# Kernel tuning notes

Measured on AMD Instinct MI355X. Metric: run time of the kernel, lower is better.

Reference implementation:

```python
import jax, jax.numpy as jnp
import numpy as np

B, H, W, C, UNITS = 16, 64, 64, 64, 128

def setup_inputs() -> dict:
    key = jax.random.key(0)
    k1, k2 = jax.random.split(key)
    x = jax.random.normal(k1, (B, H, W, C), dtype=jnp.float32)
    # 'random_normal' keras initializer defaults to stddev=0.05
    w = jax.random.normal(k2, (UNITS, C, W, H), dtype=jnp.float32) * 0.05
    return {"x": x, "w": w}

def reference(x, w):
    # Original: transpose NHWC->NCHW, broadcasted matmul (W,H)@(H,W),
    # reduce-sum over C, transpose back, relu.
    # Fused contraction: y[b,i,j,u] = sum_{c,h} w[u,c,i,h] * x[b,h,j,c]
    y = jnp.einsum('ucih,bhjc->biju', w, x)  # (B, W, W, units)
    return jax.nn.relu(y)
```

## Files before the change

### kernel.cpp

```cpp
#include <hip/hip_runtime.h>
#include <hip/hip_bf16.h>


typedef __attribute__((ext_vector_type(4))) float f32x4;
typedef __attribute__((ext_vector_type(8))) short bf16x8;
typedef __attribute__((ext_vector_type(4))) unsigned int u32x4;
typedef __attribute__((ext_vector_type(2))) unsigned int u32x2;
typedef unsigned short ushort_t;

static __device__ __forceinline__ unsigned int cvt_pk_bf16(float lo, float hi) {
  unsigned int r;
  asm("v_cvt_pk_bf16_f32 %0, %1, %2" : "=v"(r) : "v"(lo), "v"(hi));
  return r;
}

static __device__ __forceinline__ void async_copy16(void* lds, const void* g) {
  __builtin_amdgcn_global_load_lds(
      (const __attribute__((address_space(1))) unsigned int*)g,
      (__attribute__((address_space(3))) unsigned int*)lds, 16, 0, 0);
}

__global__ __launch_bounds__(256)
void conv_x(const float* __restrict__ X, ushort_t* __restrict__ Xb, int n4) {
  int idx = blockIdx.x * 256 + threadIdx.x;
  const int stride = gridDim.x * 256;
  for (; idx < n4; idx += stride) {
    f32x4 v = ((const f32x4*)X)[idx];
    u32x2 o;
    o.x = cvt_pk_bf16(v.x, v.y);
    o.y = cvt_pk_bf16(v.z, v.w);
    ((u32x2*)Xb)[idx] = o;
  }
}

__global__ __launch_bounds__(256)
void conv_w(const float* __restrict__ W, ushort_t* __restrict__ Wb) {
  __shared__ float T[64][65];
  const int bid = blockIdx.x;
  const int u = bid >> 6;
  const int i = bid & 63;
  const int t = threadIdx.x;

  const int hq = t & 15;
  const int c4 = t >> 4;
  const float* base = W + (((size_t)u * 64) * 64 + i) * 64;
#pragma unroll
  for (int it = 0; it < 4; ++it) {
    const int c = it * 16 + c4;
    f32x4 v = *(const f32x4*)(base + (size_t)c * 4096 + hq * 4);
    *(f32x4*)&T[c][hq * 4] = v;
  }
  __syncthreads();

  const int h = t >> 2;
  const int c0 = (t & 3) * 16;
  unsigned int pk[8];
#pragma unroll
  for (int q = 0; q < 8; ++q)
    pk[q] = cvt_pk_bf16(T[c0 + 2 * q][h], T[c0 + 2 * q + 1][h]);
  ushort_t* out = Wb + (((size_t)i * 128 + u) * 64 + h) * 64 + c0;
  ((u32x4*)out)[0] = *(u32x4*)&pk[0];
  ((u32x4*)out)[1] = *(u32x4*)&pk[4];
}

__global__ __launch_bounds__(512, 1)
void gemm256(const ushort_t* __restrict__ Xb, const ushort_t* __restrict__ Wb,
             float* __restrict__ P0, float* __restrict__ P1) {
  __shared__ ushort_t As[3][256 * 32];
  __shared__ ushort_t Bs[3][256 * 32];

  const int tid = threadIdx.x;
  const int lane = tid & 63;
  const int wid = tid >> 6;
  const int wm = wid >> 2;
  const int wn = wid & 3;

  const int bid = blockIdx.x;
  const int wg = (bid & 7) * 32 + (bid >> 3);
  const int mt = wg & 3;
  const int rest = wg >> 2;
  const int ks = rest & 1;
  const int nt2 = rest >> 1;

  const char* XbB = (const char*)Xb;
  const char* WbB = (const char*)Wb;
  const int kb6 = ks * 32;

  int a_dst[2]; size_t a_srcb[2];
  int b_dst[2]; size_t b_srcb[2];
#pragma unroll
  for (int it = 0; it < 2; ++it) {
    const int flat = it * 8192 + tid * 16;
    const int row = flat >> 6;
    const int p = (flat >> 4) & 3;
    const int ps = p ^ ((row >> 1) & 3);
    a_dst[it] = flat;
    a_srcb[it] = (size_t)(mt * 4 + (row >> 6)) * 524288 +
                 (size_t)(row & 63) * 128 + ps * 16;
    b_dst[it] = flat;
    b_srcb[it] = (size_t)(nt2 * 256 + row) * 8192 + ps * 16;
  }

  int a_ro[2][4], b_ro[4];
#pragma unroll
  for (int mh = 0; mh < 2; ++mh)
#pragma unroll
    for (int f = 0; f < 4; ++f) {
      const int row = wm * 128 + mh * 64 + f * 16 + (lane & 15);
      a_ro[mh][f] = row * 64 + (((lane >> 4) ^ ((row >> 1) & 3)) << 4);
    }
#pragma unroll
  for (int f = 0; f < 4; ++f) {
    const int row = wn * 64 + f * 16 + (lane & 15);
    b_ro[f] = row * 64 + (((lane >> 4) ^ ((row >> 1) & 3)) << 4);
  }

  f32x4 acc[8][4];
#pragma unroll
  for (int i = 0; i < 8; ++i)
#pragma unroll
    for (int j = 0; j < 4; ++j) acc[i][j] = (f32x4){0.f, 0.f, 0.f, 0.f};

  auto stageA = [&](int buf, int T) {
    char* la = (char*)&As[buf][0];
    const size_t koff = (size_t)(kb6 + (T >> 1)) * 8192 + (T & 1) * 64;
#pragma unroll
    for (int it = 0; it < 2; ++it)
      async_copy16(la + a_dst[it], XbB + a_srcb[it] + koff);
  };
  auto stageB = [&](int buf, int T) {
    char* lb = (char*)&Bs[buf][0];
    const size_t koff = (size_t)(kb6 + (T >> 1)) * 128 + (T & 1) * 64;
#pragma unroll
    for (int it = 0; it < 2; ++it)
      async_copy16(lb + b_dst[it], WbB + b_srcb[it] + koff);
  };

  stageA(0, 0); stageB(0, 0);
  stageA(1, 1); stageB(1, 1);
  asm volatile("s_waitcnt vmcnt(4)" ::: "memory");
  __builtin_amdgcn_s_barrier();

  int cur = 0, pre = 2;
  for (int t = 0; t < 64; ++t) {
    const char* ab = (const char*)&As[cur][0];
    const char* bb = (const char*)&Bs[cur][0];
    bf16x8 fa[4], fb[4], fa2[4];

    __builtin_amdgcn_sched_barrier(0);
#pragma unroll
    for (int f = 0; f < 4; ++f) fa[f] = *(const bf16x8*)(ab + a_ro[0][f]);
#pragma unroll
    for (int f = 0; f < 4; ++f) fb[f] = *(const bf16x8*)(bb + b_ro[f]);
    if (t + 2 < 64) stageA(pre, t + 2);
    __builtin_amdgcn_s_barrier();
    asm volatile("s_waitcnt lgkmcnt(0)" ::: "memory");
    __builtin_amdgcn_sched_barrier(0);
    __builtin_amdgcn_s_setprio(1);
#pragma unroll
    for (int f = 0; f < 4; ++f)
#pragma unroll
      for (int nf = 0; nf < 4; ++nf)
        acc[f][nf] = __builtin_amdgcn_mfma_f32_16x16x32_bf16(
            fa[f], fb[nf], acc[f][nf], 0, 0, 0);
    __builtin_amdgcn_s_setprio(0);
    __builtin_amdgcn_s_barrier();

    __builtin_amdgcn_sched_barrier(0);
#pragma unroll
    for (int f = 0; f < 4; ++f) fa2[f] = *(const bf16x8*)(ab + a_ro[1][f]);
    if (t + 2 < 64) stageB(pre, t + 2);
    __builtin_amdgcn_s_barrier();
    asm volatile("s_waitcnt lgkmcnt(0)" ::: "memory");
    __builtin_amdgcn_sched_barrier(0);
    __builtin_amdgcn_s_setprio(1);
#pragma unroll
    for (int f = 0; f < 4; ++f)
#pragma unroll
      for (int nf = 0; nf < 4; ++nf)
        acc[4 + f][nf] = __builtin_amdgcn_mfma_f32_16x16x32_bf16(
            fa2[f], fb[nf], acc[4 + f][nf], 0, 0, 0);
    __builtin_amdgcn_s_setprio(0);
    if (t < 62) {
      asm volatile("s_waitcnt vmcnt(4)" ::: "memory");
    } else if (t == 62) {
      asm volatile("s_waitcnt vmcnt(0)" ::: "memory");
    }
    __builtin_amdgcn_s_barrier();

    cur = (cur == 2) ? 0 : cur + 1;
    pre = (pre == 2) ? 0 : pre + 1;
  }

  float* P = ks ? P1 : P0;
  const int rbase = (lane >> 4) * 4;
  const int cn = lane & 15;
#pragma unroll
  for (int mf = 0; mf < 8; ++mf) {
#pragma unroll
    for (int r = 0; r < 4; ++r) {
      const int m = mt * 256 + wm * 128 + mf * 16 + rbase + r;
      const int b = m >> 6;
      const int j = m & 63;
#pragma unroll
      for (int nf = 0; nf < 4; ++nf) {
        const int nloc = wn * 64 + nf * 16 + cn;
        const int i = nt2 * 2 + (nloc >> 7);
        const int u = nloc & 127;
        P[(((size_t)b * 64 + i) * 64 + j) * 128 + u] = acc[mf][nf][r];
      }
    }
  }
}

__global__ __launch_bounds__(256)
void add_relu(float* __restrict__ Out, const float* __restrict__ P1, int n4) {
  int idx = blockIdx.x * 256 + threadIdx.x;
  const int stride = gridDim.x * 256;
  for (; idx < n4; idx += stride) {
    f32x4 a = ((const f32x4*)Out)[idx];
    f32x4 b = ((const f32x4*)P1)[idx];
    f32x4 r;
    r.x = fmaxf(a.x + b.x, 0.f);
    r.y = fmaxf(a.y + b.y, 0.f);
    r.z = fmaxf(a.z + b.z, 0.f);
    r.w = fmaxf(a.w + b.w, 0.f);
    ((f32x4*)Out)[idx] = r;
  }
}

__global__ __launch_bounds__(512, 2)
void gemm8(const ushort_t* __restrict__ Xb, const ushort_t* __restrict__ Wb,
           float* __restrict__ O) {
  __shared__ ushort_t As[3][128 * 64];
  __shared__ ushort_t Bs[3][256 * 64];

  const int tid = threadIdx.x;
  const int lane = tid & 63;
  const int wid = tid >> 6;
  const int wm = wid >> 2;
  const int wn = wid & 3;

  const int bid = blockIdx.x;
  const int wg = (bid & 7) * 32 + (bid >> 3);
  const int mt = wg & 7;
  const int nt2 = wg >> 3;

  const char* XbB = (const char*)Xb;
  const char* WbB = (const char*)Wb;

  int a_dst[2]; size_t a_src[2];
#pragma unroll
  for (int it = 0; it < 2; ++it) {
    const int flat = it * 8192 + tid * 16;
    const int row = flat >> 7;
    const int p = (flat >> 4) & 7;
    const int b = mt * 2 + (row >> 6);
    const int j = row & 63;
    a_dst[it] = flat;
    a_src[it] = (size_t)b * 524288 + (size_t)j * 128 + ((p ^ (row & 7)) << 4);
  }
  int b_dst[4]; size_t b_src[4];
#pragma unroll
  for (int it = 0; it < 4; ++it) {
    const int flat = it * 8192 + tid * 16;
    const int nl = flat >> 7;
    const int p = (flat >> 4) & 7;
    b_dst[it] = flat;
    b_src[it] = (size_t)(nt2 * 256 + nl) * 8192 + ((p ^ (nl & 7)) << 4);
  }

  int a_ro[2][4], b_ro[2][4];
#pragma unroll
  for (int kk = 0; kk < 2; ++kk) {
#pragma unroll
    for (int f = 0; f < 4; ++f) {
      int row = wm * 64 + f * 16 + (lane & 15);
      int byte0 = row * 128 + kk * 64 + (lane >> 4) * 16;
      a_ro[kk][f] = byte0 ^ ((row & 7) << 4);
      row = wn * 64 + f * 16 + (lane & 15);
      byte0 = row * 128 + kk * 64 + (lane >> 4) * 16;
      b_ro[kk][f] = byte0 ^ ((row & 7) << 4);
    }
  }

  f32x4 acc[4][4];
#pragma unroll
  for (int i = 0; i < 4; ++i)
#pragma unroll
    for (int j = 0; j < 4; ++j) acc[i][j] = (f32x4){0.f, 0.f, 0.f, 0.f};

  auto stage = [&](int buf, int h) {
    char* la = (char*)&As[buf][0];
    char* lb = (char*)&Bs[buf][0];
#pragma unroll
    for (int it = 0; it < 2; ++it)
      async_copy16(la + a_dst[it], XbB + a_src[it] + (size_t)h * 8192);
#pragma unroll
    for (int it = 0; it < 4; ++it)
      async_copy16(lb + b_dst[it], WbB + b_src[it] + (size_t)h * 128);
  };
  auto stage3a = [&](int buf, int h) {
    char* la = (char*)&As[buf][0];
    char* lb = (char*)&Bs[buf][0];
#pragma unroll
    for (int it = 0; it < 2; ++it)
      async_copy16(la + a_dst[it], XbB + a_src[it] + (size_t)h * 8192);
    async_copy16(lb + b_dst[0], WbB + b_src[0] + (size_t)h * 128);
  };
  auto stage3b = [&](int buf, int h) {
    char* lb = (char*)&Bs[buf][0];
#pragma unroll
    for (int it = 1; it < 4; ++it)
      async_copy16(lb + b_dst[it], WbB + b_src[it] + (size_t)h * 128);
  };

  bf16x8 fa0[4], fb0[4], fa1[4], fb1[4];
  auto readFrags = [&](bf16x8 (&fa)[4], bf16x8 (&fb)[4], int buf, int kk) {
    const char* ab = (const char*)&As[buf][0];
    const char* bb = (const char*)&Bs[buf][0];
#pragma unroll
    for (int f = 0; f < 4; ++f) fa[f] = *(const bf16x8*)(ab + a_ro[kk][f]);
#pragma unroll
    for (int f = 0; f < 4; ++f) fb[f] = *(const bf16x8*)(bb + b_ro[kk][f]);
  };

  stage(0, 0);
  stage(1, 1);
  asm volatile("s_waitcnt vmcnt(6)" ::: "memory");
  __builtin_amdgcn_s_barrier();
  readFrags(fa0, fb0, 0, 0);

  int cur = 0, nxt = 1, pre = 2;
  for (int t = 0; t < 64; ++t) {
    __builtin_amdgcn_sched_barrier(0);
    readFrags(fa1, fb1, cur, 1);
    if (t + 2 < 64) stage3a(pre, t + 2);
    if (t < 62) {
      asm volatile("s_waitcnt vmcnt(3)" ::: "memory");
    } else {
      asm volatile("s_waitcnt vmcnt(0)" ::: "memory");
    }
    __builtin_amdgcn_sched_barrier(0);
    __builtin_amdgcn_s_barrier();
    __builtin_amdgcn_s_setprio(1);
#pragma unroll
    for (int mf = 0; mf < 4; ++mf)
#pragma unroll
      for (int nf = 0; nf < 4; ++nf)
        acc[mf][nf] = __builtin_amdgcn_mfma_f32_16x16x32_bf16(
            fa0[mf], fb0[nf], acc[mf][nf], 0, 0, 0);
    __builtin_amdgcn_s_setprio(0);
    __builtin_amdgcn_s_barrier();

    __builtin_amdgcn_sched_barrier(0);
    if (t + 1 < 64) readFrags(fa0, fb0, nxt, 0);
    if (t + 2 < 64) stage3b(pre, t + 2);
    __builtin_amdgcn_sched_barrier(0);
    __builtin_amdgcn_s_barrier();
    __builtin_amdgcn_s_setprio(1);
#pragma unroll
    for (int mf = 0; mf < 4; ++mf)
#pragma unroll
      for (int nf = 0; nf < 4; ++nf)
        acc[mf][nf] = __builtin_amdgcn_mfma_f32_16x16x32_bf16(
            fa1[mf], fb1[nf], acc[mf][nf], 0, 0, 0);
    __builtin_amdgcn_s_setprio(0);
    __builtin_amdgcn_s_barrier();

    cur = (cur == 2) ? 0 : cur + 1;
    nxt = (nxt == 2) ? 0 : nxt + 1;
    pre = (pre == 2) ? 0 : pre + 1;
  }

  const int rbase = (lane >> 4) * 4;
  const int cn = lane & 15;
#pragma unroll
  for (int mf = 0; mf < 4; ++mf) {
#pragma unroll
    for (int r = 0; r < 4; ++r) {
      const int ml = wm * 64 + mf * 16 + rbase + r;
      const int m = mt * 128 + ml;
      const int b = m >> 6;
      const int j = m & 63;
#pragma unroll
      for (int nf = 0; nf < 4; ++nf) {
        const int nloc = wn * 64 + nf * 16 + cn;
        const int i = nt2 * 2 + (nloc >> 7);
        const int u = nloc & 127;
        O[(((size_t)b * 64 + i) * 64 + j) * 128 + u] = fmaxf(acc[mf][nf][r], 0.f);
      }
    }
  }
}

__global__ __launch_bounds__(256, 2)
void fused_gemm(const float* __restrict__ X, const float* __restrict__ Wt,
                float* __restrict__ O) {
  __shared__ ushort_t As[2][128 * 64];
  __shared__ ushort_t Bs[2][128 * 64];
  const int tid = threadIdx.x;
  const int lane = tid & 63;
  const int wid = tid >> 6;
  const int wm = wid >> 1;
  const int wn = wid & 1;
  const int bid = blockIdx.x;
  const int wg = (bid & 7) * 64 + (bid >> 3);
  const int mt = wg & 7;
  const int nt = wg >> 3;
  const int a_ml = tid >> 1;
  const int a_hp = (tid & 1) * 2;
  const int a_b = (mt * 128 + a_ml) >> 6;
  const int a_j = a_ml & 63;
  const float* a_base = X + ((size_t)a_b << 18) + ((size_t)a_j << 6);
  const int b_nl = tid >> 1;
  const int b_c8 = (tid & 1) * 8;
  const float* b_base = Wt + ((size_t)b_nl << 18) + ((size_t)nt << 6);
  f32x4 ra[2][4];
  f32x4 rb[8];
  f32x4 acc[4][4];
#pragma unroll
  for (int i = 0; i < 4; ++i)
#pragma unroll
    for (int j = 0; j < 4; ++j) acc[i][j] = (f32x4){0.f, 0.f, 0.f, 0.f};
  auto stage_load = [&](int t) {
    const int th = t & 15;
    const int tc = t >> 4;
    const int c0 = tc * 16;
    const int h0 = th * 4;
#pragma unroll
    for (int s = 0; s < 2; ++s) {
      const float* p = a_base + (size_t)(h0 + a_hp + s) * 4096 + c0;
#pragma unroll
      for (int q = 0; q < 4; ++q) ra[s][q] = ((const f32x4*)p)[q];
    }
#pragma unroll
    for (int q = 0; q < 8; ++q)
      rb[q] = *(const f32x4*)(b_base + (size_t)(c0 + b_c8 + q) * 4096 + h0);
  };
  auto stage_write = [&](int buf) {
    char* abase = (char*)&As[buf][0];
    const int swa = (a_ml & 7) << 4;
#pragma unroll
    for (int s = 0; s < 2; ++s) {
      u32x4 lo, hi;
      lo.x = cvt_pk_bf16(ra[s][0].x, ra[s][0].y);
      lo.y = cvt_pk_bf16(ra[s][0].z, ra[s][0].w);
      lo.z = cvt_pk_bf16(ra[s][1].x, ra[s][1].y);
      lo.w = cvt_pk_bf16(ra[s][1].z, ra[s][1].w);
      hi.x = cvt_pk_bf16(ra[s][2].x, ra[s][2].y);
      hi.y = cvt_pk_bf16(ra[s][2].z, ra[s][2].w);
      hi.z = cvt_pk_bf16(ra[s][3].x, ra[s][3].y);
      hi.w = cvt_pk_bf16(ra[s][3].z, ra[s][3].w);
      const int byte0 = a_ml * 128 + (a_hp + s) * 32;
      *(u32x4*)(abase + (byte0 ^ swa)) = lo;
      *(u32x4*)(abase + ((byte0 + 16) ^ swa)) = hi;
    }
    char* bbase = (char*)&Bs[buf][0];
    const int swb = (b_nl & 7) << 4;
#pragma unroll
    for (int hl = 0; hl < 4; ++hl) {
      u32x4 v;
      v.x = cvt_pk_bf16(rb[0][hl], rb[1][hl]);
      v.y = cvt_pk_bf16(rb[2][hl], rb[3][hl]);
      v.z = cvt_pk_bf16(rb[4][hl], rb[5][hl]);
      v.w = cvt_pk_bf16(rb[6][hl], rb[7][hl]);
      const int byte0 = b_nl * 128 + (hl * 16 + b_c8) * 2;
      *(u32x4*)(bbase + (byte0 ^ swb)) = v;
    }
  };
  auto compute = [&](int buf) {
    const char* abase = (const char*)&As[buf][0];
    const char* bbase = (const char*)&Bs[buf][0];
#pragma unroll
    for (int kk = 0; kk < 2; ++kk) {
      bf16x8 af[4], bfr[4];
#pragma unroll
      for (int mf = 0; mf < 4; ++mf) {
        const int row = wm * 64 + mf * 16 + (lane & 15);
        const int byte0 = row * 128 + kk * 64 + (lane >> 4) * 16;
        af[mf] = *(const bf16x8*)(abase + (byte0 ^ ((row & 7) << 4)));
      }
#pragma unroll
      for (int nf = 0; nf < 4; ++nf) {
        const int row = wn * 64 + nf * 16 + (lane & 15);
        const int byte0 = row * 128 + kk * 64 + (lane >> 4) * 16;
        bfr[nf] = *(const bf16x8*)(bbase + (byte0 ^ ((row & 7) << 4)));
      }
#pragma unroll
      for (int mf = 0; mf < 4; ++mf)
#pragma unroll
        for (int nf = 0; nf < 4; ++nf)
          acc[mf][nf] = __builtin_amdgcn_mfma_f32_16x16x32_bf16(
              af[mf], bfr[nf], acc[mf][nf], 0, 0, 0);
    }
  };
  stage_load(0);
  stage_write(0);
  __syncthreads();
  int cur = 0;
  for (int t = 0; t < 64; ++t) {
    if (t + 1 < 64) stage_load(t + 1);
    compute(cur);
    if (t + 1 < 64) stage_write(cur ^ 1);
    __syncthreads();
    cur ^= 1;
  }
  const int rbase = (lane >> 4) * 4;
  const int cn = lane & 15;
#pragma unroll
  for (int mf = 0; mf < 4; ++mf) {
#pragma unroll
    for (int r = 0; r < 4; ++r) {
      const int ml = wm * 64 + mf * 16 + rbase + r;
      const int m = mt * 128 + ml;
      const int b = m >> 6;
      const int j = m & 63;
      float* orow = O + (((size_t)b * 64 + nt) * 64 + j) * 128;
#pragma unroll
      for (int nf = 0; nf < 4; ++nf) {
        const int u = wn * 64 + nf * 16 + cn;
        orow[u] = fmaxf(acc[mf][nf][r], 0.f);
      }
    }
  }
}

extern "C" void kernel_launch(void* const* d_in, const int* in_sizes, int n_in,
                              void* d_out, int out_size, void* d_ws, size_t ws_size,
                              hipStream_t stream) {
  const float* x = (const float*)d_in[0];
  const float* w = (const float*)d_in[1];
  float* out = (float*)d_out;

  const size_t XB_BYTES = (size_t)16 * 64 * 64 * 64 * 2;
  const size_t WB_BYTES = (size_t)64 * 128 * 64 * 64 * 2;
  const size_t P1_BYTES = (size_t)16 * 64 * 64 * 128 * 4;

  if (ws_size >= XB_BYTES + WB_BYTES + P1_BYTES) {
    ushort_t* Xb = (ushort_t*)d_ws;
    ushort_t* Wb = (ushort_t*)((char*)d_ws + XB_BYTES);
    float* P1 = (float*)((char*)d_ws + XB_BYTES + WB_BYTES);
    hipLaunchKernelGGL(conv_x, dim3(1024), dim3(256), 0, stream, x, Xb,
                       (int)(16 * 64 * 64 * 64 / 4));
    hipLaunchKernelGGL(conv_w, dim3(8192), dim3(256), 0, stream, w, Wb);
    hipLaunchKernelGGL(gemm256, dim3(256), dim3(512), 0, stream, Xb, Wb, out, P1);
    hipLaunchKernelGGL(add_relu, dim3(2048), dim3(256), 0, stream, out, P1,
                       (int)(16 * 64 * 64 * 128 / 4));
  } else if (ws_size >= XB_BYTES + WB_BYTES) {
    ushort_t* Xb = (ushort_t*)d_ws;
    ushort_t* Wb = (ushort_t*)((char*)d_ws + XB_BYTES);
    hipLaunchKernelGGL(conv_x, dim3(1024), dim3(256), 0, stream, x, Xb,
                       (int)(16 * 64 * 64 * 64 / 4));
    hipLaunchKernelGGL(conv_w, dim3(8192), dim3(256), 0, stream, w, Wb);
    hipLaunchKernelGGL(gemm8, dim3(256), dim3(512), 0, stream, Xb, Wb, out);
  } else {
    hipLaunchKernelGGL(fused_gemm, dim3(512), dim3(256), 0, stream, x, w, out);
  }
}
```

Before: 132.0 us.

## Store split-K partials as bf16 and deepen GEMM K-tile with double buffering

The split-K GEMM now writes both partial results to bf16 workspace buffers instead of fp32, and a new reduction kernel adds them and applies relu while writing fp32 output. This roughly halves the partial-sum write and read traffic, at the cost of rounding each partial to bf16 before the sum, which loosens accuracy. The GEMM main loop is also restructured to use 64-wide K tiles with a two-buffer pipeline, an 8-way XOR swizzle and half as many iterations. In exchange it waits for all outstanding loads (vmcnt 0) at the end of every iteration.

```diff
diff --git a/kernel.cpp b/kernel.cpp
--- a/kernel.cpp
+++ b/kernel.cpp
@@ -12,6 +12,11 @@
   unsigned int r;
   asm("v_cvt_pk_bf16_f32 %0, %1, %2" : "=v"(r) : "v"(lo), "v"(hi));
   return r;
+}
+
+static __device__ __forceinline__ float bf2f(ushort_t u) {
+  unsigned int v = ((unsigned int)u) << 16;
+  return __builtin_bit_cast(float, v);
 }
 
 static __device__ __forceinline__ void async_copy16(void* lds, const void* g) {
@@ -64,10 +69,10 @@
 }
 
 __global__ __launch_bounds__(512, 1)
-void gemm256(const ushort_t* __restrict__ Xb, const ushort_t* __restrict__ Wb,
-             float* __restrict__ P0, float* __restrict__ P1) {
-  __shared__ ushort_t As[3][256 * 32];
-  __shared__ ushort_t Bs[3][256 * 32];
+void gemm256k(const ushort_t* __restrict__ Xb, const ushort_t* __restrict__ Wb,
+              ushort_t* __restrict__ P0, ushort_t* __restrict__ P1) {
+  __shared__ ushort_t As[2][256 * 64];
+  __shared__ ushort_t Bs[2][256 * 64];
 
   const int tid = threadIdx.x;
   const int lane = tid & 63;
@@ -78,41 +83,43 @@
   const int bid = blockIdx.x;
   const int wg = (bid & 7) * 32 + (bid >> 3);
   const int mt = wg & 3;
-  const int rest = wg >> 2;
-  const int ks = rest & 1;
-  const int nt2 = rest >> 1;
+  const int ks = (wg >> 2) & 1;
+  const int nt2 = wg >> 3;
+  const int h0 = ks * 32;
 
   const char* XbB = (const char*)Xb;
   const char* WbB = (const char*)Wb;
-  const int kb6 = ks * 32;
-
-  int a_dst[2]; size_t a_srcb[2];
-  int b_dst[2]; size_t b_srcb[2];
-#pragma unroll
-  for (int it = 0; it < 2; ++it) {
+
+  int a_dst[4]; size_t a_src[4];
+  int b_dst[4]; size_t b_src[4];
+#pragma unroll
+  for (int it = 0; it < 4; ++it) {
     const int flat = it * 8192 + tid * 16;
-    const int row = flat >> 6;
-    const int p = (flat >> 4) & 3;
-    const int ps = p ^ ((row >> 1) & 3);
+    const int row = flat >> 7;
+    const int p = (flat >> 4) & 7;
+    const int ps = p ^ (row & 7);
     a_dst[it] = flat;
-    a_srcb[it] = (size_t)(mt * 4 + (row >> 6)) * 524288 +
-                 (size_t)(row & 63) * 128 + ps * 16;
+    a_src[it] = (size_t)(mt * 4 + (row >> 6)) * 524288 +
+                (size_t)(row & 63) * 128 + ps * 16;
     b_dst[it] = flat;
-    b_srcb[it] = (size_t)(nt2 * 256 + row) * 8192 + ps * 16;
-  }
-
-  int a_ro[2][4], b_ro[4];
-#pragma unroll
-  for (int mh = 0; mh < 2; ++mh)
+    b_src[it] = (size_t)(nt2 * 256 + row) * 8192 + ps * 16;
+  }
+
+  int a_ro[2][8], b_ro[2][4];
+#pragma unroll
+  for (int kk = 0; kk < 2; ++kk) {
+#pragma unroll
+    for (int f = 0; f < 8; ++f) {
+      const int row = wm * 128 + f * 16 + (lane & 15);
+      const int byte0 = row * 128 + kk * 64 + (lane >> 4) * 16;
+      a_ro[kk][f] = byte0 ^ ((row & 7) << 4);
+    }
 #pragma unroll
     for (int f = 0; f < 4; ++f) {
-      const int row = wm * 128 + mh * 64 + f * 16 + (lane & 15);
-      a_ro[mh][f] = row * 64 + (((lane >> 4) ^ ((row >> 1) & 3)) << 4);
-    }
-#pragma unroll
-  for (int f = 0; f < 4; ++f) {
-    const int row = wn * 64 + f * 16 + (lane & 15);
-    b_ro[f] = row * 64 + (((lane >> 4) ^ ((row >> 1) & 3)) << 4);
+      const int row = wn * 64 + f * 16 + (lane & 15);
+      const int byte0 = row * 128 + kk * 64 + (lane >> 4) * 16;
+      b_ro[kk][f] = byte0 ^ ((row & 7) << 4);
+    }
   }
 
   f32x4 acc[8][4];
@@ -121,78 +128,68 @@
 #pragma unroll
     for (int j = 0; j < 4; ++j) acc[i][j] = (f32x4){0.f, 0.f, 0.f, 0.f};
 
-  auto stageA = [&](int buf, int T) {
+  auto stage = [&](int buf, int t) {
     char* la = (char*)&As[buf][0];
-    const size_t koff = (size_t)(kb6 + (T >> 1)) * 8192 + (T & 1) * 64;
-#pragma unroll
-    for (int it = 0; it < 2; ++it)
-      async_copy16(la + a_dst[it], XbB + a_srcb[it] + koff);
-  };
-  auto stageB = [&](int buf, int T) {
     char* lb = (char*)&Bs[buf][0];
-    const size_t koff = (size_t)(kb6 + (T >> 1)) * 128 + (T & 1) * 64;
-#pragma unroll
-    for (int it = 0; it < 2; ++it)
-      async_copy16(lb + b_dst[it], WbB + b_srcb[it] + koff);
-  };
-
-  stageA(0, 0); stageB(0, 0);
-  stageA(1, 1); stageB(1, 1);
-  asm volatile("s_waitcnt vmcnt(4)" ::: "memory");
+    const size_t ha = (size_t)(h0 + t) * 8192;
+    const size_t hb = (size_t)(h0 + t) * 128;
+#pragma unroll
+    for (int it = 0; it < 4; ++it)
+      async_copy16(la + a_dst[it], XbB + a_src[it] + ha);
+#pragma unroll
+    for (int it = 0; it < 4; ++it)
+      async_copy16(lb + b_dst[it], WbB + b_src[it] + hb);
+  };
+
+  stage(0, 0);
+  asm volatile("s_waitcnt vmcnt(0)" ::: "memory");
   __builtin_amdgcn_s_barrier();
 
-  int cur = 0, pre = 2;
-  for (int t = 0; t < 64; ++t) {
+  int cur = 0;
+  for (int t = 0; t < 32; ++t) {
     const char* ab = (const char*)&As[cur][0];
     const char* bb = (const char*)&Bs[cur][0];
-    bf16x8 fa[4], fb[4], fa2[4];
-
-    __builtin_amdgcn_sched_barrier(0);
-#pragma unroll
-    for (int f = 0; f < 4; ++f) fa[f] = *(const bf16x8*)(ab + a_ro[0][f]);
-#pragma unroll
-    for (int f = 0; f < 4; ++f) fb[f] = *(const bf16x8*)(bb + b_ro[f]);
-    if (t + 2 < 64) stageA(pre, t + 2);
-    __builtin_amdgcn_s_barrier();
-    asm volatile("s_waitcnt lgkmcnt(0)" ::: "memory");
-    __builtin_amdgcn_sched_barrier(0);
+    bf16x8 fa[8], fb[4];
+
+    __builtin_amdgcn_sched_barrier(0);
+#pragma unroll
+    for (int f = 0; f < 8; ++f) fa[f] = *(const bf16x8*)(ab + a_ro[0][f]);
+#pragma unroll
+    for (int f = 0; f < 4; ++f) fb[f] = *(const bf16x8*)(bb + b_ro[0][f]);
+    if (t + 1 < 32) stage(cur ^ 1, t + 1);
+    __builtin_amdgcn_sched_barrier(0);
+    __builtin_amdgcn_s_barrier();
     __builtin_amdgcn_s_setprio(1);
 #pragma unroll
-    for (int f = 0; f < 4; ++f)
+    for (int mf = 0; mf < 8; ++mf)
 #pragma unroll
       for (int nf = 0; nf < 4; ++nf)
-        acc[f][nf] = __builtin_amdgcn_mfma_f32_16x16x32_bf16(
-            fa[f], fb[nf], acc[f][nf], 0, 0, 0);
+        acc[mf][nf] = __builtin_amdgcn_mfma_f32_16x16x32_bf16(
+            fa[mf], fb[nf], acc[mf][nf], 0, 0, 0);
     __builtin_amdgcn_s_setprio(0);
     __builtin_amdgcn_s_barrier();
 
     __builtin_amdgcn_sched_barrier(0);
 #pragma unroll
-    for (int f = 0; f < 4; ++f) fa2[f] = *(const bf16x8*)(ab + a_ro[1][f]);
-    if (t + 2 < 64) stageB(pre, t + 2);
-    __builtin_amdgcn_s_barrier();
-    asm volatile("s_waitcnt lgkmcnt(0)" ::: "memory");
-    __builtin_amdgcn_sched_barrier(0);
+    for (int f = 0; f < 8; ++f) fa[f] = *(const bf16x8*)(ab + a_ro[1][f]);
+#pragma unroll
+    for (int f = 0; f < 4; ++f) fb[f] = *(const bf16x8*)(bb + b_ro[1][f]);
+    __builtin_amdgcn_sched_barrier(0);
+    __builtin_amdgcn_s_barrier();
     __builtin_amdgcn_s_setprio(1);
 #pragma unroll
-    for (int f = 0; f < 4; ++f)
+    for (int mf = 0; mf < 8; ++mf)
 #pragma unroll
       for (int nf = 0; nf < 4; ++nf)
-        acc[4 + f][nf] = __builtin_amdgcn_mfma_f32_16x16x32_bf16(
-            fa2[f], fb[nf], acc[4 + f][nf], 0, 0, 0);
+        acc[mf][nf] = __builtin_amdgcn_mfma_f32_16x16x32_bf16(
+            fa[mf], fb[nf], acc[mf][nf], 0, 0, 0);
     __builtin_amdgcn_s_setprio(0);
-    if (t < 62) {
-      asm volatile("s_waitcnt vmcnt(4)" ::: "memory");
-    } else if (t == 62) {
-      asm volatile("s_waitcnt vmcnt(0)" ::: "memory");
-    }
-    __builtin_amdgcn_s_barrier();
-
-    cur = (cur == 2) ? 0 : cur + 1;
-    pre = (pre == 2) ? 0 : pre + 1;
-  }
-
-  float* P = ks ? P1 : P0;
+    asm volatile("s_waitcnt vmcnt(0)" ::: "memory");
+    __builtin_amdgcn_s_barrier();
+    cur ^= 1;
+  }
+
+  ushort_t* P = ks ? P1 : P0;
   const int rbase = (lane >> 4) * 4;
   const int cn = lane & 15;
 #pragma unroll
@@ -207,26 +204,28 @@
         const int nloc = wn * 64 + nf * 16 + cn;
         const int i = nt2 * 2 + (nloc >> 7);
         const int u = nloc & 127;
-        P[(((size_t)b * 64 + i) * 64 + j) * 128 + u] = acc[mf][nf][r];
+        P[(((size_t)b * 64 + i) * 64 + j) * 128 + u] =
+            (ushort_t)(cvt_pk_bf16(acc[mf][nf][r], 0.f) & 0xffff);
       }
     }
   }
 }
 
 __global__ __launch_bounds__(256)
-void add_relu(float* __restrict__ Out, const float* __restrict__ P1, int n4) {
-  int idx = blockIdx.x * 256 + threadIdx.x;
-  const int stride = gridDim.x * 256;
-  for (; idx < n4; idx += stride) {
-    f32x4 a = ((const f32x4*)Out)[idx];
-    f32x4 b = ((const f32x4*)P1)[idx];
-    f32x4 r;
-    r.x = fmaxf(a.x + b.x, 0.f);
-    r.y = fmaxf(a.y + b.y, 0.f);
-    r.z = fmaxf(a.z + b.z, 0.f);
-    r.w = fmaxf(a.w + b.w, 0.f);
-    ((f32x4*)Out)[idx] = r;
-  }
+void add_relu_bf(const ushort_t* __restrict__ P0, const ushort_t* __restrict__ P1,
+                 float* __restrict__ Out, int n8) {
+  const int idx = blockIdx.x * 256 + threadIdx.x;
+  if (idx >= n8) return;
+  bf16x8 a = ((const bf16x8*)P0)[idx];
+  bf16x8 b = ((const bf16x8*)P1)[idx];
+  f32x4 o0, o1;
+#pragma unroll
+  for (int k = 0; k < 4; ++k) {
+    o0[k] = fmaxf(bf2f((ushort_t)a[k]) + bf2f((ushort_t)b[k]), 0.f);
+    o1[k] = fmaxf(bf2f((ushort_t)a[4 + k]) + bf2f((ushort_t)b[4 + k]), 0.f);
+  }
+  ((f32x4*)Out)[2 * idx] = o0;
+  ((f32x4*)Out)[2 * idx + 1] = o1;
 }
 
 __global__ __launch_bounds__(512, 2)
@@ -535,18 +534,19 @@
 
   const size_t XB_BYTES = (size_t)16 * 64 * 64 * 64 * 2;
   const size_t WB_BYTES = (size_t)64 * 128 * 64 * 64 * 2;
-  const size_t P1_BYTES = (size_t)16 * 64 * 64 * 128 * 4;
-
-  if (ws_size >= XB_BYTES + WB_BYTES + P1_BYTES) {
+  const size_t PB_BYTES = (size_t)16 * 64 * 64 * 128 * 2;
+
+  if (ws_size >= XB_BYTES + WB_BYTES + 2 * PB_BYTES) {
     ushort_t* Xb = (ushort_t*)d_ws;
     ushort_t* Wb = (ushort_t*)((char*)d_ws + XB_BYTES);
-    float* P1 = (float*)((char*)d_ws + XB_BYTES + WB_BYTES);
+    ushort_t* P0 = (ushort_t*)((char*)d_ws + XB_BYTES + WB_BYTES);
+    ushort_t* P1 = (ushort_t*)((char*)d_ws + XB_BYTES + WB_BYTES + PB_BYTES);
     hipLaunchKernelGGL(conv_x, dim3(1024), dim3(256), 0, stream, x, Xb,
                        (int)(16 * 64 * 64 * 64 / 4));
     hipLaunchKernelGGL(conv_w, dim3(8192), dim3(256), 0, stream, w, Wb);
-    hipLaunchKernelGGL(gemm256, dim3(256), dim3(512), 0, stream, Xb, Wb, out, P1);
-    hipLaunchKernelGGL(add_relu, dim3(2048), dim3(256), 0, stream, out, P1,
-                       (int)(16 * 64 * 64 * 128 / 4));
+    hipLaunchKernelGGL(gemm256k, dim3(256), dim3(512), 0, stream, Xb, Wb, P0, P1);
+    hipLaunchKernelGGL(add_relu_bf, dim3(4096), dim3(256), 0, stream, P0, P1,
+                       out, (int)(16 * 64 * 64 * 128 / 8));
   } else if (ws_size >= XB_BYTES + WB_BYTES) {
     ushort_t* Xb = (ushort_t*)d_ws;
     ushort_t* Wb = (ushort_t*)((char*)d_ws + XB_BYTES);
```

Measured after the change: 120.1 us. -9.0%, faster.
